# Performance work log

Hardware: AMD Instinct MI355X
Metric: run time of the kernel (lower is better)

The kernel has to match this reference:

```python
import jax, jax.numpy as jnp
import numpy as np


def _laplacian(A):
    # D^{-1/2} A D^{-1/2}; original builds diag matrices and does D@A@D,
    # which is mathematically identical to broadcast row/col scaling.
    d = jnp.sum(A, axis=-1)
    dinv = 1.0 / jnp.sqrt(d)
    return A * dinv[:, None] * dinv[None, :]


def _poly(A, theta):
    # P = I + sum_{i=1..k} theta_sig[i-1] * A^i  (theta passed through sigmoid)
    t = jax.nn.sigmoid(theta)
    N = A.shape[-1]
    P = jnp.eye(N, dtype=A.dtype)
    seg = P
    for i in range(theta.shape[0]):  # k is small (2), static loop over poly order
        seg = seg @ A
        P = P + seg * t[i]
    return P


def setup_inputs() -> dict:
    key = jax.random.key(0)
    k1, k2, k3, k4 = jax.random.split(key, 4)
    N, DIN, DOUT, K_CHEB = 4096, 64, 64, 2
    return {
        "x": jax.random.normal(k1, (N, DIN), dtype=jnp.float32),
        "A": jax.random.uniform(k2, (N, N), dtype=jnp.float32),  # positive row sums
        "theta": jax.random.normal(k3, (K_CHEB,), dtype=jnp.float32),
        "W": jax.random.normal(k4, (DOUT, DIN), dtype=jnp.float32) / np.float32(np.sqrt(DIN)),
        "b": jnp.zeros((DOUT,), dtype=jnp.float32),
        "k": 4,
    }


def reference(x, A, theta, W, b, k):
    S = _laplacian(A)
    S = _poly(S, theta)
    S = _laplacian(S)
    # double argsort over last dim = per-row descending rank of each entry
    rank = jnp.argsort(jnp.argsort(-S, axis=-1), axis=-1)
    mask = jnp.where(rank < k, jnp.float32(1.0), jnp.float32(0.0))
    S = S * mask  # keep only top-k entries per row
    x = S @ x     # [N,N] @ [N,DIN]
    return x @ W.T + b  # nn.Linear
```

## Files before the change

### kernel.cpp

```cpp
#include <hip/hip_runtime.h>
#include <hip/hip_bf16.h>
#include <float.h>
#include <math.h>

#define N 4096
#define DIN 64

typedef signed char i8_t;
typedef signed char i8x4 __attribute__((ext_vector_type(4)));
typedef int i32x4 __attribute__((ext_vector_type(4)));
typedef float f32x4 __attribute__((ext_vector_type(4)));

__device__ __forceinline__ void gload16(const void* g, void* l) {
    __builtin_amdgcn_global_load_lds((const __attribute__((address_space(1))) void*)g,
                                     (__attribute__((address_space(3))) void*)l,
                                     16, 0, 0);
}

__device__ __forceinline__ float block_reduce_sum(float s) {
    __shared__ float red[4];
    #pragma unroll
    for (int off = 32; off; off >>= 1) s += __shfl_down(s, off);
    if ((threadIdx.x & 63) == 0) red[threadIdx.x >> 6] = s;
    __syncthreads();
    return red[0] + red[1] + red[2] + red[3];
}

__device__ __forceinline__ bool better(float v1, int j1, float v2, int j2) {
    return v1 > v2 || (v1 == v2 && j1 < j2);
}
__device__ __forceinline__ void ins4(float v, int j, float bv[4], int bj[4]) {
    if (!better(v, j, bv[3], bj[3])) return;
    bv[3] = v; bj[3] = j;
    if (better(bv[3], bj[3], bv[2], bj[2])) {
        float tv = bv[2]; int tj = bj[2]; bv[2] = bv[3]; bj[2] = bj[3]; bv[3] = tv; bj[3] = tj;
    }
    if (better(bv[2], bj[2], bv[1], bj[1])) {
        float tv = bv[1]; int tj = bj[1]; bv[1] = bv[2]; bj[1] = bj[2]; bv[2] = tv; bj[2] = tj;
    }
    if (better(bv[1], bj[1], bv[0], bj[0])) {
        float tv = bv[0]; int tj = bj[0]; bv[0] = bv[1]; bj[0] = bj[1]; bv[1] = tv; bj[1] = tj;
    }
}

__global__ __launch_bounds__(256) void k_rowsum_dinv(const float* __restrict__ A,
                                                     float* __restrict__ dinv,
                                                     float* __restrict__ rowsumP) {
    int row = blockIdx.x, tid = threadIdx.x;
    const float4* a4 = (const float4*)(A + (size_t)row * N);
    float s = 0.f;
    for (int j = tid; j < N / 4; j += 256) {
        float4 v = a4[j];
        s += v.x + v.y + v.z + v.w;
    }
    float tot = block_reduce_sum(s);
    if (tid == 0) {
        dinv[row] = rsqrtf(tot);
        rowsumP[row] = 0.f;
    }
}

__global__ __launch_bounds__(1024) void k_dmax(const float* __restrict__ dinv,
                                               float* __restrict__ dmaxf) {
    int t = threadIdx.x;
    float m = fmaxf(fmaxf(dinv[t], dinv[t + 1024]), fmaxf(dinv[t + 2048], dinv[t + 3072]));
    #pragma unroll
    for (int off = 32; off; off >>= 1) m = fmaxf(m, __shfl_down(m, off));
    __shared__ float red[16];
    if ((t & 63) == 0) red[t >> 6] = m;
    __syncthreads();
    if (t == 0) {
        float mm = red[0];
        #pragma unroll
        for (int i = 1; i < 16; i++) mm = fmaxf(mm, red[i]);
        *dmaxf = mm;
    }
}

__global__ __launch_bounds__(256) void k_make_sqt(const float* __restrict__ A,
                                                  const float* __restrict__ dinv,
                                                  const float* __restrict__ dmaxf,
                                                  i8_t* __restrict__ Sq,
                                                  i8_t* __restrict__ Tq) {
    __shared__ float tile[64][65];
    int tid = threadIdx.x;
    int c4 = tid & 15;
    int rg = tid >> 4;
    int i0 = blockIdx.y * 64;
    int j0 = blockIdx.x * 64;
    float dmax = *dmaxf;
    float sinv = 127.0f / (dmax * dmax);
    float4 dj = *(const float4*)(dinv + j0 + 4 * c4);
    #pragma unroll
    for (int rr = 0; rr < 4; rr++) {
        int r = rg + 16 * rr;
        int row = i0 + r;
        float di = dinv[row];
        float4 av = *(const float4*)(A + (size_t)row * N + j0 + 4 * c4);
        float s0 = av.x * di * dj.x, s1 = av.y * di * dj.y;
        float s2 = av.z * di * dj.z, s3 = av.w * di * dj.w;
        i8x4 qv;
        qv[0] = (i8_t)(int)fminf(rintf(s0 * sinv), 127.f);
        qv[1] = (i8_t)(int)fminf(rintf(s1 * sinv), 127.f);
        qv[2] = (i8_t)(int)fminf(rintf(s2 * sinv), 127.f);
        qv[3] = (i8_t)(int)fminf(rintf(s3 * sinv), 127.f);
        *(i8x4*)(Sq + (size_t)row * N + j0 + 4 * c4) = qv;
        tile[r][4 * c4 + 0] = s0;
        tile[r][4 * c4 + 1] = s1;
        tile[r][4 * c4 + 2] = s2;
        tile[r][4 * c4 + 3] = s3;
    }
    __syncthreads();
    #pragma unroll
    for (int cc = 0; cc < 4; cc++) {
        int c = rg + 16 * cc;
        int gj = j0 + c;
        i8x4 qv;
        #pragma unroll
        for (int u = 0; u < 4; u++)
            qv[u] = (i8_t)(int)fminf(rintf(tile[4 * c4 + u][c] * sinv), 127.f);
        *(i8x4*)(Tq + (size_t)gj * N + i0 + 4 * c4) = qv;
    }
}

__global__ __launch_bounds__(256) void k_xw(const float* __restrict__ x,
                                            const float* __restrict__ W,
                                            float* __restrict__ XW) {
    __shared__ float Wl[64][65];
    __shared__ float xs[4][64];
    int tid = threadIdx.x;
    for (int i = tid; i < 64 * 64; i += 256) Wl[i >> 6][i & 63] = W[i];
    int r = tid >> 6, o = tid & 63;
    int row = blockIdx.x * 4 + r;
    xs[r][o] = x[(size_t)row * DIN + o];
    __syncthreads();
    float acc = 0.f;
    #pragma unroll
    for (int d = 0; d < 64; d++) acc += xs[r][d] * Wl[o][d];
    XW[(size_t)row * DIN + o] = acc;
}

__global__ __launch_bounds__(256) void k_gemm(const i8_t* __restrict__ Sq,
                                              const i8_t* __restrict__ Tq,
                                              const float* __restrict__ dmaxf,
                                              const float* __restrict__ theta,
                                              float* __restrict__ rowsumP,
                                              float* __restrict__ candV,
                                              int* __restrict__ candJ) {
    __shared__ __attribute__((aligned(64))) float pbuf[128][65];
    i8_t* const smem = (i8_t*)pbuf;

    int tid = threadIdx.x;
    int lane = tid & 63;
    int wave = tid >> 6;
    int wr = wave >> 1, wc = wave & 1;

    int bid = blockIdx.x;
    int xcd = bid & 7, local = bid >> 3;
    int bi = ((xcd & 1) << 4) + (local & 15);
    int bj = ((xcd >> 1) << 3) + (local >> 4);

    int qoff = ((tid & 3) ^ ((tid >> 3) & 3)) * 16;
    int row0 = tid >> 2;
    const i8_t* Ag0 = Sq + (size_t)(bi * 128 + row0) * N + qoff;
    const i8_t* Ag1 = Sq + (size_t)(bi * 128 + 64 + row0) * N + qoff;
    const i8_t* Bg0 = Tq + (size_t)(bj * 128 + row0) * N + qoff;
    const i8_t* Bg1 = Tq + (size_t)(bj * 128 + 64 + row0) * N + qoff;
    int l0 = tid * 16;
    int l1 = (tid + 256) * 16;

    i32x4 acc[4][4];
    i32x4 z = {0, 0, 0, 0};
    #pragma unroll
    for (int i = 0; i < 4; i++)
        #pragma unroll
        for (int j = 0; j < 4; j++) acc[i][j] = z;

    int r = lane & 15, q = lane >> 4;
    int qs = q ^ ((r >> 1) & 3);
    int aoff = (wr * 64 + r) * 64 + qs * 16;
    int boff = (wc * 64 + r) * 64 + qs * 16;

    gload16(Ag0, smem + l0);
    gload16(Ag1, smem + l1);
    gload16(Bg0, smem + 8192 + l0);
    gload16(Bg1, smem + 8192 + l1);

    int p = 0;
    for (int t = 0; t < N / 64; ++t) {
        int k1 = (t + 1) * 64;
        if (k1 < N) {
            i8_t* d = smem + (p ^ 1) * 16384;
            gload16(Ag0 + k1, d + l0);
            gload16(Ag1 + k1, d + l1);
            gload16(Bg0 + k1, d + 8192 + l0);
            gload16(Bg1 + k1, d + 8192 + l1);
            asm volatile("s_waitcnt vmcnt(4)" ::: "memory");
        } else {
            asm volatile("s_waitcnt vmcnt(0)" ::: "memory");
        }
        __builtin_amdgcn_s_barrier();

        const i8_t* Ab = smem + p * 16384;
        const i8_t* Bb = Ab + 8192;
        i32x4 af[4], bfr[4];
        #pragma unroll
        for (int mi = 0; mi < 4; mi++) af[mi] = *(const i32x4*)(Ab + aoff + mi * 16 * 64);
        #pragma unroll
        for (int ni = 0; ni < 4; ni++) bfr[ni] = *(const i32x4*)(Bb + boff + ni * 16 * 64);

        __builtin_amdgcn_s_setprio(1);
        #pragma unroll
        for (int mi = 0; mi < 4; mi++)
            #pragma unroll
            for (int ni = 0; ni < 4; ni++)
                acc[mi][ni] = __builtin_amdgcn_mfma_i32_16x16x64_i8(af[mi], bfr[ni],
                                                                    acc[mi][ni], 0, 0, 0);
        __builtin_amdgcn_s_setprio(0);

        asm volatile("s_waitcnt lgkmcnt(0)" ::: "memory");
        __builtin_amdgcn_s_barrier();
        p ^= 1;
    }

    float dmax = *dmaxf;
    float sq = dmax * dmax / 127.0f;
    float t0 = 1.f / (1.f + expf(-theta[0]));
    float t1 = 1.f / (1.f + expf(-theta[1]));
    float t0s = t0 * sq;
    float t1s2 = t1 * sq * sq;
    int col = lane & 15, quad = lane >> 4;

    #pragma unroll
    for (int mi = 0; mi < 4; mi++) {
        int gi0 = bi * 128 + wr * 64 + mi * 16 + quad * 4;
        float rsum[4] = {0.f, 0.f, 0.f, 0.f};
        #pragma unroll
        for (int ni = 0; ni < 4; ni++) {
            int gj = bj * 128 + wc * 64 + ni * 16 + col;
            f32x4 pf;
            #pragma unroll
            for (int rr = 0; rr < 4; rr++) {
                int gi = gi0 + rr;
                float qv = (float)Sq[(size_t)gi * N + gj];
                float p2 = t1s2 * (float)acc[mi][ni][rr] + t0s * qv + ((gi == gj) ? 1.f : 0.f);
                pf[rr] = p2;
                rsum[rr] += p2;
            }
            acc[mi][ni] = __builtin_bit_cast(i32x4, pf);
        }
        #pragma unroll
        for (int rr = 0; rr < 4; rr++) {
            float v = rsum[rr];
            v += __shfl_xor(v, 1);
            v += __shfl_xor(v, 2);
            v += __shfl_xor(v, 4);
            v += __shfl_xor(v, 8);
            if (col == 0) atomicAdd(&rowsumP[gi0 + rr], v);
        }
    }

    float bv[4] = {-FLT_MAX, -FLT_MAX, -FLT_MAX, -FLT_MAX};
    int bjx[4] = {N, N, N, N};
    int srow = tid >> 1;
    int shalf = tid & 1;

    #pragma unroll
    for (int pass = 0; pass < 2; pass++) {
        if (wc == pass) {
            #pragma unroll
            for (int mi = 0; mi < 4; mi++) {
                int prow = wr * 64 + mi * 16 + quad * 4;
                #pragma unroll
                for (int ni = 0; ni < 4; ni++) {
                    f32x4 pf = __builtin_bit_cast(f32x4, acc[mi][ni]);
                    #pragma unroll
                    for (int rr = 0; rr < 4; rr++)
                        pbuf[prow + rr][ni * 16 + col] = pf[rr];
                }
            }
        }
        __syncthreads();
        int jbase = bj * 128 + pass * 64 + shalf * 32;
        for (int i = 0; i < 32; i++)
            ins4(pbuf[srow][shalf * 32 + i], jbase + i, bv, bjx);
        __syncthreads();
    }

    float ov[4]; int oj[4];
    #pragma unroll
    for (int c = 0; c < 4; c++) { ov[c] = __shfl_xor(bv[c], 1); oj[c] = __shfl_xor(bjx[c], 1); }
    #pragma unroll
    for (int c = 0; c < 4; c++) ins4(ov[c], oj[c], bv, bjx);
    if (shalf == 0) {
        size_t base = ((size_t)(bi * 128 + srow) * 32 + bj) * 4;
        #pragma unroll
        for (int c = 0; c < 4; c++) { candV[base + c] = bv[c]; candJ[base + c] = bjx[c]; }
    }
}

__global__ __launch_bounds__(256) void k_dinv2(const float* __restrict__ rowsumP,
                                               float* __restrict__ dinv2) {
    int g = blockIdx.x * 256 + threadIdx.x;
    dinv2[g] = rsqrtf(rowsumP[g]);
}

__global__ __launch_bounds__(64) void k_final(const float* __restrict__ candV,
                                              const int* __restrict__ candJ,
                                              const float* __restrict__ dinv2,
                                              const float* __restrict__ XW,
                                              const float* __restrict__ bvec,
                                              const int* __restrict__ kin,
                                              float* __restrict__ out) {
    int row = blockIdx.x, t = threadIdx.x;
    float2 cv = *(const float2*)(candV + (size_t)row * 128 + t * 2);
    int2 cj = *(const int2*)(candJ + (size_t)row * 128 + t * 2);
    float bv[4] = {-FLT_MAX, -FLT_MAX, -FLT_MAX, -FLT_MAX};
    int bj[4] = {N, N, N, N};
    ins4(cv.x * dinv2[cj.x], cj.x, bv, bj);
    ins4(cv.y * dinv2[cj.y], cj.y, bv, bj);
    #pragma unroll
    for (int off = 1; off < 64; off <<= 1) {
        float ov[4]; int oj[4];
        #pragma unroll
        for (int c = 0; c < 4; c++) { ov[c] = __shfl_xor(bv[c], off); oj[c] = __shfl_xor(bj[c], off); }
        #pragma unroll
        for (int c = 0; c < 4; c++) ins4(ov[c], oj[c], bv, bj);
    }
    int kk = kin[0];
    if (kk > 4) kk = 4;
    if (kk < 0) kk = 0;
    float sc = dinv2[row];
    float o = bvec[t];
    for (int c = 0; c < kk; c++)
        o += sc * bv[c] * XW[(size_t)bj[c] * DIN + t];
    out[(size_t)row * DIN + t] = o;
}

extern "C" void kernel_launch(void* const* d_in, const int* in_sizes, int n_in,
                              void* d_out, int out_size, void* d_ws, size_t ws_size,
                              hipStream_t stream) {
    const float* x = (const float*)d_in[0];
    const float* A = (const float*)d_in[1];
    const float* theta = (const float*)d_in[2];
    const float* W = (const float*)d_in[3];
    const float* b = (const float*)d_in[4];
    const int* kin = (const int*)d_in[5];
    float* out = (float*)d_out;

    char* ws = (char*)d_ws;
    i8_t* Sq = (i8_t*)ws;
    i8_t* Tq = (i8_t*)(ws + (size_t)N * N);
    float* candV = (float*)(ws + (size_t)N * N * 2);
    int* candJ = (int*)(ws + (size_t)N * N * 2 + (size_t)N * 128 * 4);
    float* dinv = (float*)(ws + (size_t)N * N * 2 + (size_t)N * 128 * 8);
    float* dinv2 = dinv + N;
    float* rowsumP = dinv2 + N;
    float* dmaxf = rowsumP + N;
    float* XW = (float*)(ws + (size_t)N * N * 2 + (size_t)N * 128 * 8 + 65536);

    k_xw<<<N / 4, 256, 0, stream>>>(x, W, XW);
    k_rowsum_dinv<<<N, 256, 0, stream>>>(A, dinv, rowsumP);
    k_dmax<<<1, 1024, 0, stream>>>(dinv, dmaxf);
    k_make_sqt<<<dim3(64, 64), 256, 0, stream>>>(A, dinv, dmaxf, Sq, Tq);
    k_gemm<<<1024, 256, 0, stream>>>(Sq, Tq, dmaxf, theta, rowsumP, candV, candJ);
    k_dinv2<<<N / 256, 256, 0, stream>>>(rowsumP, dinv2);
    k_final<<<N, 64, 0, stream>>>(candV, candJ, dinv2, XW, b, kin, out);
}
```

Baseline: 252.3 us.

## Enlarge int8 GEMM tile to 256x256 with 8 waves and rework top-k candidate pass

The int8 MFMA GEMM moves from 128x128 tiles with 4 waves to 256x256 tiles with 8 waves, each wave holding an 8x4 accumulator grid. This halves global and LDS traffic per output and cuts the grid to 256 blocks, one per CU. The per-tile top-4 selection now runs in four 64-row passes, with 8 threads per row and a shuffle merge. Each row then produces 16 candidate groups instead of 32, which shrinks the candidate buffers and the final merge. The cost is more accumulator registers (launch bounds 512,2) and a single-wave grid that could leave tail imbalance or pressure occupancy.

Result: slower. 261.6 us (+3.7%).

```diff
diff --git a/kernel.cpp b/kernel.cpp
--- a/kernel.cpp
+++ b/kernel.cpp
@@ -140,78 +140,79 @@
     XW[(size_t)row * DIN + o] = acc;
 }
 
-__global__ __launch_bounds__(256) void k_gemm(const i8_t* __restrict__ Sq,
-                                              const i8_t* __restrict__ Tq,
-                                              const float* __restrict__ dmaxf,
-                                              const float* __restrict__ theta,
-                                              float* __restrict__ rowsumP,
-                                              float* __restrict__ candV,
-                                              int* __restrict__ candJ) {
-    __shared__ __attribute__((aligned(64))) float pbuf[128][65];
+__global__ __launch_bounds__(512, 2) void k_gemm(const i8_t* __restrict__ Sq,
+                                                 const i8_t* __restrict__ Tq,
+                                                 const float* __restrict__ dmaxf,
+                                                 const float* __restrict__ theta,
+                                                 float* __restrict__ rowsumP,
+                                                 float* __restrict__ candV,
+                                                 int* __restrict__ candJ) {
+    __shared__ __attribute__((aligned(128))) float pbuf[64][264];
     i8_t* const smem = (i8_t*)pbuf;
 
     int tid = threadIdx.x;
     int lane = tid & 63;
     int wave = tid >> 6;
-    int wr = wave >> 1, wc = wave & 1;
+    int wr = wave >> 2;
+    int wc = wave & 3;
 
     int bid = blockIdx.x;
     int xcd = bid & 7, local = bid >> 3;
-    int bi = ((xcd & 1) << 4) + (local & 15);
-    int bj = ((xcd >> 1) << 3) + (local >> 4);
+    int bi = ((xcd & 1) << 3) + (local & 7);
+    int bj = ((xcd >> 1) << 2) + (local >> 3);
 
     int qoff = ((tid & 3) ^ ((tid >> 3) & 3)) * 16;
     int row0 = tid >> 2;
-    const i8_t* Ag0 = Sq + (size_t)(bi * 128 + row0) * N + qoff;
-    const i8_t* Ag1 = Sq + (size_t)(bi * 128 + 64 + row0) * N + qoff;
-    const i8_t* Bg0 = Tq + (size_t)(bj * 128 + row0) * N + qoff;
-    const i8_t* Bg1 = Tq + (size_t)(bj * 128 + 64 + row0) * N + qoff;
+    const i8_t* Ag0 = Sq + (size_t)(bi * 256 + row0) * N + qoff;
+    const i8_t* Ag1 = Sq + (size_t)(bi * 256 + 128 + row0) * N + qoff;
+    const i8_t* Bg0 = Tq + (size_t)(bj * 256 + row0) * N + qoff;
+    const i8_t* Bg1 = Tq + (size_t)(bj * 256 + 128 + row0) * N + qoff;
     int l0 = tid * 16;
-    int l1 = (tid + 256) * 16;
-
-    i32x4 acc[4][4];
+    int l1 = (tid + 512) * 16;
+
+    i32x4 acc[8][4];
     i32x4 z = {0, 0, 0, 0};
     #pragma unroll
-    for (int i = 0; i < 4; i++)
+    for (int i = 0; i < 8; i++)
         #pragma unroll
         for (int j = 0; j < 4; j++) acc[i][j] = z;
 
     int r = lane & 15, q = lane >> 4;
     int qs = q ^ ((r >> 1) & 3);
-    int aoff = (wr * 64 + r) * 64 + qs * 16;
+    int aoff = (wr * 128 + r) * 64 + qs * 16;
     int boff = (wc * 64 + r) * 64 + qs * 16;
 
     gload16(Ag0, smem + l0);
     gload16(Ag1, smem + l1);
-    gload16(Bg0, smem + 8192 + l0);
-    gload16(Bg1, smem + 8192 + l1);
+    gload16(Bg0, smem + 16384 + l0);
+    gload16(Bg1, smem + 16384 + l1);
 
     int p = 0;
     for (int t = 0; t < N / 64; ++t) {
         int k1 = (t + 1) * 64;
         if (k1 < N) {
-            i8_t* d = smem + (p ^ 1) * 16384;
+            i8_t* d = smem + (p ^ 1) * 32768;
             gload16(Ag0 + k1, d + l0);
             gload16(Ag1 + k1, d + l1);
-            gload16(Bg0 + k1, d + 8192 + l0);
-            gload16(Bg1 + k1, d + 8192 + l1);
+            gload16(Bg0 + k1, d + 16384 + l0);
+            gload16(Bg1 + k1, d + 16384 + l1);
             asm volatile("s_waitcnt vmcnt(4)" ::: "memory");
         } else {
             asm volatile("s_waitcnt vmcnt(0)" ::: "memory");
         }
         __builtin_amdgcn_s_barrier();
 
-        const i8_t* Ab = smem + p * 16384;
-        const i8_t* Bb = Ab + 8192;
-        i32x4 af[4], bfr[4];
-        #pragma unroll
-        for (int mi = 0; mi < 4; mi++) af[mi] = *(const i32x4*)(Ab + aoff + mi * 16 * 64);
+        const i8_t* Ab = smem + p * 32768;
+        const i8_t* Bb = Ab + 16384;
+        i32x4 af[8], bfr[4];
+        #pragma unroll
+        for (int mi = 0; mi < 8; mi++) af[mi] = *(const i32x4*)(Ab + aoff + mi * 16 * 64);
         #pragma unroll
         for (int ni = 0; ni < 4; ni++) bfr[ni] = *(const i32x4*)(Bb + boff + ni * 16 * 64);
 
         __builtin_amdgcn_s_setprio(1);
         #pragma unroll
-        for (int mi = 0; mi < 4; mi++)
+        for (int mi = 0; mi < 8; mi++)
             #pragma unroll
             for (int ni = 0; ni < 4; ni++)
                 acc[mi][ni] = __builtin_amdgcn_mfma_i32_16x16x64_i8(af[mi], bfr[ni],
@@ -232,12 +233,12 @@
     int col = lane & 15, quad = lane >> 4;
 
     #pragma unroll
-    for (int mi = 0; mi < 4; mi++) {
-        int gi0 = bi * 128 + wr * 64 + mi * 16 + quad * 4;
+    for (int mi = 0; mi < 8; mi++) {
+        int gi0 = bi * 256 + wr * 128 + mi * 16 + quad * 4;
         float rsum[4] = {0.f, 0.f, 0.f, 0.f};
         #pragma unroll
         for (int ni = 0; ni < 4; ni++) {
-            int gj = bj * 128 + wc * 64 + ni * 16 + col;
+            int gj = bj * 256 + wc * 64 + ni * 16 + col;
             f32x4 pf;
             #pragma unroll
             for (int rr = 0; rr < 4; rr++) {
@@ -260,42 +261,47 @@
         }
     }
 
-    float bv[4] = {-FLT_MAX, -FLT_MAX, -FLT_MAX, -FLT_MAX};
-    int bjx[4] = {N, N, N, N};
-    int srow = tid >> 1;
-    int shalf = tid & 1;
-
-    #pragma unroll
-    for (int pass = 0; pass < 2; pass++) {
-        if (wc == pass) {
-            #pragma unroll
-            for (int mi = 0; mi < 4; mi++) {
-                int prow = wr * 64 + mi * 16 + quad * 4;
+    int srow = tid >> 3;
+    int sub = tid & 7;
+    __syncthreads();
+
+    #pragma unroll
+    for (int pass = 0; pass < 4; pass++) {
+        if (wr == (pass >> 1)) {
+            int mi0 = (pass & 1) * 4;
+            #pragma unroll
+            for (int m2 = 0; m2 < 4; m2++) {
                 #pragma unroll
                 for (int ni = 0; ni < 4; ni++) {
-                    f32x4 pf = __builtin_bit_cast(f32x4, acc[mi][ni]);
+                    f32x4 pf = __builtin_bit_cast(f32x4, acc[mi0 + m2][ni]);
                     #pragma unroll
                     for (int rr = 0; rr < 4; rr++)
-                        pbuf[prow + rr][ni * 16 + col] = pf[rr];
+                        pbuf[m2 * 16 + quad * 4 + rr][wc * 64 + ni * 16 + col] = pf[rr];
                 }
             }
         }
         __syncthreads();
-        int jbase = bj * 128 + pass * 64 + shalf * 32;
-        for (int i = 0; i < 32; i++)
-            ins4(pbuf[srow][shalf * 32 + i], jbase + i, bv, bjx);
+        float bv[4] = {-FLT_MAX, -FLT_MAX, -FLT_MAX, -FLT_MAX};
+        int bjx[4] = {N, N, N, N};
+        int jbase = bj * 256;
+        for (int i = 0; i < 32; i++) {
+            int c = i * 8 + sub;
+            ins4(pbuf[srow][c], jbase + c, bv, bjx);
+        }
+        #pragma unroll
+        for (int off = 1; off < 8; off <<= 1) {
+            float ov[4]; int oj[4];
+            #pragma unroll
+            for (int c = 0; c < 4; c++) { ov[c] = __shfl_xor(bv[c], off); oj[c] = __shfl_xor(bjx[c], off); }
+            #pragma unroll
+            for (int c = 0; c < 4; c++) ins4(ov[c], oj[c], bv, bjx);
+        }
+        if (sub == 0) {
+            size_t base = ((size_t)(bi * 256 + pass * 64 + srow) * 16 + bj) * 4;
+            #pragma unroll
+            for (int c = 0; c < 4; c++) { candV[base + c] = bv[c]; candJ[base + c] = bjx[c]; }
+        }
         __syncthreads();
-    }
-
-    float ov[4]; int oj[4];
-    #pragma unroll
-    for (int c = 0; c < 4; c++) { ov[c] = __shfl_xor(bv[c], 1); oj[c] = __shfl_xor(bjx[c], 1); }
-    #pragma unroll
-    for (int c = 0; c < 4; c++) ins4(ov[c], oj[c], bv, bjx);
-    if (shalf == 0) {
-        size_t base = ((size_t)(bi * 128 + srow) * 32 + bj) * 4;
-        #pragma unroll
-        for (int c = 0; c < 4; c++) { candV[base + c] = bv[c]; candJ[base + c] = bjx[c]; }
     }
 }
 
@@ -313,12 +319,11 @@
                                               const int* __restrict__ kin,
                                               float* __restrict__ out) {
     int row = blockIdx.x, t = threadIdx.x;
-    float2 cv = *(const float2*)(candV + (size_t)row * 128 + t * 2);
-    int2 cj = *(const int2*)(candJ + (size_t)row * 128 + t * 2);
+    float cv = candV[(size_t)row * 64 + t];
+    int cj = candJ[(size_t)row * 64 + t];
     float bv[4] = {-FLT_MAX, -FLT_MAX, -FLT_MAX, -FLT_MAX};
     int bj[4] = {N, N, N, N};
-    ins4(cv.x * dinv2[cj.x], cj.x, bv, bj);
-    ins4(cv.y * dinv2[cj.y], cj.y, bv, bj);
+    ins4(cv * dinv2[cj], cj, bv, bj);
     #pragma unroll
     for (int off = 1; off < 64; off <<= 1) {
         float ov[4]; int oj[4];
@@ -352,18 +357,18 @@
     i8_t* Sq = (i8_t*)ws;
     i8_t* Tq = (i8_t*)(ws + (size_t)N * N);
     float* candV = (float*)(ws + (size_t)N * N * 2);
-    int* candJ = (int*)(ws + (size_t)N * N * 2 + (size_t)N * 128 * 4);
-    float* dinv = (float*)(ws + (size_t)N * N * 2 + (size_t)N * 128 * 8);
+    int* candJ = (int*)(ws + (size_t)N * N * 2 + (size_t)N * 64 * 4);
+    float* dinv = (float*)(ws + (size_t)N * N * 2 + (size_t)N * 64 * 8);
     float* dinv2 = dinv + N;
     float* rowsumP = dinv2 + N;
     float* dmaxf = rowsumP + N;
-    float* XW = (float*)(ws + (size_t)N * N * 2 + (size_t)N * 128 * 8 + 65536);
+    float* XW = (float*)(ws + (size_t)N * N * 2 + (size_t)N * 64 * 8 + 65536);
 
     k_xw<<<N / 4, 256, 0, stream>>>(x, W, XW);
     k_rowsum_dinv<<<N, 256, 0, stream>>>(A, dinv, rowsumP);
     k_dmax<<<1, 1024, 0, stream>>>(dinv, dmaxf);
     k_make_sqt<<<dim3(64, 64), 256, 0, stream>>>(A, dinv, dmaxf, Sq, Tq);
-    k_gemm<<<1024, 256, 0, stream>>>(Sq, Tq, dmaxf, theta, rowsumP, candV, candJ);
+    k_gemm<<<256, 512, 0, stream>>>(Sq, Tq, dmaxf, theta, rowsumP, candV, candJ);
     k_dinv2<<<N / 256, 256, 0, stream>>>(rowsumP, dinv2);
     k_final<<<N, 64, 0, stream>>>(candV, candJ, dinv2, XW, b, kin, out);
 }
```
